# Kernel optimization log

Measured on AMD Instinct MI355X. Metric: run time of the kernel, lower is better.

## Reference

```python
import jax, jax.numpy as jnp
import numpy as np

N = 50000          # nodes
E = 1_600_000      # directed edges (before self loops)
G = 128            # graphs in batch
IN_F = 64
C1, H = 32, 4      # gat1: out_channels=32, heads=4 -> hidden 128
C2 = 64            # gat2: out_channels=64, heads=1, concat=False
OUT_F = 2
EPS = 1e-5
NEG_SLOPE = 0.2    # PyG GATv2Conv default


def setup_inputs() -> dict:
    key = jax.random.key(0)
    ks = jax.random.split(key, 24)
    s = 0.05
    inp = {
        'x': jax.random.normal(ks[0], (N, IN_F), jnp.float32),
        'edge_index': jax.random.randint(ks[1], (2, E), 0, N, dtype=jnp.int64),
        'batch': jnp.sort(jax.random.randint(ks[2], (N,), 0, G, dtype=jnp.int64)),
        # GATv2 layer 1 (in=64 -> 4 heads x 32)
        'W1l': jax.random.normal(ks[3], (IN_F, H * C1), jnp.float32) * s,
        'b1l': jnp.zeros((H * C1,), jnp.float32),
        'W1r': jax.random.normal(ks[4], (IN_F, H * C1), jnp.float32) * s,
        'b1r': jnp.zeros((H * C1,), jnp.float32),
        'att1': jax.random.normal(ks[5], (H, C1), jnp.float32) * s,
        'bias1': jnp.zeros((H * C1,), jnp.float32),
        # GATv2 layer 2 (in=128 -> 1 head x 64, no concat)
        'W2l': jax.random.normal(ks[6], (H * C1, C2), jnp.float32) * s,
        'b2l': jnp.zeros((C2,), jnp.float32),
        'W2r': jax.random.normal(ks[7], (H * C1, C2), jnp.float32) * s,
        'b2r': jnp.zeros((C2,), jnp.float32),
        'att2': jax.random.normal(ks[8], (1, C2), jnp.float32) * s,
        'bias2': jnp.zeros((C2,), jnp.float32),
        # batchnorms (batch-statistics normalization)
        'bn1_g': jnp.ones((H * C1,), jnp.float32),
        'bn1_b': jnp.zeros((H * C1,), jnp.float32),
        'bn2_g': jnp.ones((C2,), jnp.float32),
        'bn2_b': jnp.zeros((C2,), jnp.float32),
        # final linear: CL2_F*3 -> out_f
        'lin_w': jax.random.normal(ks[9], (3 * C2, OUT_F), jnp.float32) * s,
        'lin_b': jnp.zeros((OUT_F,), jnp.float32),
    }
    return inp


def _gatv2(x, Wl, bl, Wr, br, att, bias, src, dst, heads, ch, concat, n_nodes):
    # x: [N, F_in]; src/dst: [E'] (self loops already appended)
    xl = (x @ Wl + bl).reshape(n_nodes, heads, ch)  # source transform
    xr = (x @ Wr + br).reshape(n_nodes, heads, ch)  # target transform
    m = jax.nn.leaky_relu(xl[src] + xr[dst], NEG_SLOPE)      # [E', H, C]
    logits = jnp.einsum('ehc,hc->eh', m, att)                # [E', H]
    # segment softmax over destination nodes (every node has a self loop)
    mx = jax.ops.segment_max(logits, dst, num_segments=n_nodes)
    a = jnp.exp(logits - mx[dst])
    denom = jax.ops.segment_sum(a, dst, num_segments=n_nodes)
    alpha = a / denom[dst]                                   # [E', H]
    out = jax.ops.segment_sum(xl[src] * alpha[..., None], dst,
                              num_segments=n_nodes)          # [N, H, C]
    if concat:
        out = out.reshape(n_nodes, heads * ch)
    else:
        out = out.mean(axis=1)
    return out + bias


def _bn(h, gamma, beta):
    mu = h.mean(axis=0)
    var = h.var(axis=0)
    return (h - mu) * jax.lax.rsqrt(var + EPS) * gamma + beta


def reference(x, edge_index, batch, W1l, b1l, W1r, b1r, att1, bias1,
              W2l, b2l, W2r, b2r, att2, bias2,
              bn1_g, bn1_b, bn2_g, bn2_b, lin_w, lin_b):
    n = x.shape[0]
    loops = jnp.arange(n, dtype=edge_index.dtype)
    src = jnp.concatenate([edge_index[0], loops])  # PyG add_self_loops=True
    dst = jnp.concatenate([edge_index[1], loops])

    h = jax.nn.relu(_gatv2(x, W1l, b1l, W1r, b1r, att1, bias1,
                           src, dst, H, C1, True, n))
    h = _bn(h, bn1_g, bn1_b)      # dropout is identity (eval)
    h = jax.nn.relu(_gatv2(h, W2l, b2l, W2r, b2r, att2, bias2,
                           src, dst, 1, C2, False, n))
    h = _bn(h, bn2_g, bn2_b)

    x0 = jax.ops.segment_sum(h, batch, num_segments=G)                  # add pool
    cnt = jax.ops.segment_sum(jnp.ones((n, 1), h.dtype), batch, num_segments=G)
    x1 = x0 / jnp.maximum(cnt, 1.0)                                     # mean pool
    x2 = jax.ops.segment_max(h, batch, num_segments=G)                  # max pool
    feat = jnp.concatenate([x0, x1, x2], axis=-1)                       # [G, 3*C2]
    return feat @ lin_w + lin_b
```

## Files before the change

kernel.cpp:

```cpp
#include <hip/hip_runtime.h>
#include <hip/hip_fp16.h>
#include <math.h>

#define BSHIFT 7
#define CHUNK  8192
#define CAP    6144

__device__ inline __half2 habs2_(__half2 x){
  union { __half2 h; unsigned u; } c; c.h = x; c.u &= 0x7FFF7FFFu; return c.h;
}
__device__ inline __half2 lrelu2_(__half2 x, __half2 c06, __half2 c04){
  return __hfma2(c04, habs2_(x), __hmul2(c06, x));
}

__global__ __launch_bounds__(256) void k_pre(const int* __restrict__ ei, int E, int N, int NB,
    int* __restrict__ bfill, unsigned* __restrict__ ebuf,
    const float* __restrict__ X,
    const float* __restrict__ Wl, const float* __restrict__ bl,
    const float* __restrict__ Wr, const float* __restrict__ br,
    __half* __restrict__ outl, __half* __restrict__ outr, int bb){
  __shared__ float xs[32][64];
  if ((int)blockIdx.x < bb){
    int* hist = (int*)&xs[0][0];
    int base = blockIdx.x*CHUNK;
    int EL = E + N;
    int end = min(base + CHUNK, EL);
    for (int i = threadIdx.x; i < NB; i += 256) hist[i] = 0;
    __syncthreads();
    for (int e = base + threadIdx.x; e < end; e += 256){
      int d = (e < E) ? ei[E + e] : (e - E);
      atomicAdd(&hist[d >> BSHIFT], 1);
    }
    __syncthreads();
    for (int b = threadIdx.x; b < NB; b += 256){
      int c = hist[b];
      hist[b] = (c > 0) ? (b*CAP + atomicAdd(&bfill[b], c)) : 0;
    }
    __syncthreads();
    for (int e = base + threadIdx.x; e < end; e += 256){
      int s, d;
      if (e < E){ s = ei[e]; d = ei[E + e]; } else { s = d = e - E; }
      int pos = atomicAdd(&hist[d >> BSHIFT], 1);
      ebuf[pos] = (unsigned)s | ((unsigned)d << 16);
    }
  } else {
    const int tid = threadIdx.x;
    const int n0 = ((int)blockIdx.x - bb)*32;
    for (int t = tid; t < 32*64; t += 256){
      int r = t >> 6, c = t & 63;
      int node = n0 + r;
      xs[r][c] = (node < N) ? X[(size_t)node*64 + c] : 0.f;
    }
    __syncthreads();
    const int jg = tid & 63;
    const int ng = tid >> 6;
    const int q  = jg*4;
    const bool isL = (q < 128);
    const float* W = isL ? Wl : Wr;
    const int jj   = isL ? q : q - 128;
    const float* bbp = isL ? bl : br;
    __half* OUT    = isL ? outl : outr;
    const float4 bias4 = *(const float4*)(bbp + jj);
    float acc[8][4];
    #pragma unroll
    for (int n = 0; n < 8; ++n){ acc[n][0]=acc[n][1]=acc[n][2]=acc[n][3]=0.f; }
    for (int k = 0; k < 64; k += 4){
      const float4 w0 = *(const float4*)(W + (size_t)(k+0)*128 + jj);
      const float4 w1 = *(const float4*)(W + (size_t)(k+1)*128 + jj);
      const float4 w2 = *(const float4*)(W + (size_t)(k+2)*128 + jj);
      const float4 w3 = *(const float4*)(W + (size_t)(k+3)*128 + jj);
      #pragma unroll
      for (int n = 0; n < 8; ++n){
        const float4 xv = *(const float4*)(&xs[ng*8 + n][k]);
        acc[n][0] = fmaf(xv.w,w3.x, fmaf(xv.z,w2.x, fmaf(xv.y,w1.x, fmaf(xv.x,w0.x, acc[n][0]))));
        acc[n][1] = fmaf(xv.w,w3.y, fmaf(xv.z,w2.y, fmaf(xv.y,w1.y, fmaf(xv.x,w0.y, acc[n][1]))));
        acc[n][2] = fmaf(xv.w,w3.z, fmaf(xv.z,w2.z, fmaf(xv.y,w1.z, fmaf(xv.x,w0.z, acc[n][2]))));
        acc[n][3] = fmaf(xv.w,w3.w, fmaf(xv.z,w2.w, fmaf(xv.y,w1.w, fmaf(xv.x,w0.w, acc[n][3]))));
      }
    }
    #pragma unroll
    for (int n = 0; n < 8; ++n){
      int node = n0 + ng*8 + n;
      if (node < N){
        union { __half2 h[2]; uint2 u; } cv;
        cv.h[0] = __floats2half2_rn(acc[n][0]+bias4.x, acc[n][1]+bias4.y);
        cv.h[1] = __floats2half2_rn(acc[n][2]+bias4.z, acc[n][3]+bias4.w);
        *(uint2*)(OUT + (size_t)node*128 + jj) = cv.u;
      }
    }
  }
}

__global__ __launch_bounds__(1024) void k_fine(const unsigned* __restrict__ ebuf,
    const int* __restrict__ bfill, int N, int NB,
    int* __restrict__ rstart, int* __restrict__ rend, int* __restrict__ esrc){
  __shared__ int cnt[128];
  __shared__ int sc[128];
  __shared__ int base[128];
  int b = blockIdx.x;
  int n0 = b << BSHIFT;
  int nn = min(128, N - n0);
  int e0 = b*CAP;
  int e1 = e0 + bfill[b];
  if (threadIdx.x < 128) cnt[threadIdx.x] = 0;
  __syncthreads();
  for (int e = e0 + threadIdx.x; e < e1; e += 1024)
    atomicAdd(&cnt[(ebuf[e] >> 16) & 127], 1);
  __syncthreads();
  if (threadIdx.x < 128) sc[threadIdx.x] = cnt[threadIdx.x];
  __syncthreads();
  for (int off = 1; off < 128; off <<= 1){
    int v = 0;
    if (threadIdx.x < 128 && (int)threadIdx.x >= off) v = sc[threadIdx.x - off];
    __syncthreads();
    if (threadIdx.x < 128) sc[threadIdx.x] += v;
    __syncthreads();
  }
  if (threadIdx.x < 128){
    int bs = e0 + sc[threadIdx.x] - cnt[threadIdx.x];
    base[threadIdx.x] = bs;
    if ((int)threadIdx.x < nn){
      rstart[n0 + threadIdx.x] = bs;
      rend[n0 + threadIdx.x]   = bs + cnt[threadIdx.x];
    }
    cnt[threadIdx.x] = 0;
  }
  __syncthreads();
  for (int e = e0 + threadIdx.x; e < e1; e += 1024){
    unsigned pk = ebuf[e];
    int local = (int)(pk >> 16) & 127;
    int pos = base[local] + atomicAdd(&cnt[local], 1);
    esrc[pos] = (int)(pk & 0xffffu);
  }
}

__global__ __launch_bounds__(256) void k_gemm2(const __half2* __restrict__ X2,
    const float* __restrict__ Wl, const float* __restrict__ bl,
    const float* __restrict__ Wr, const float* __restrict__ br,
    __half* __restrict__ outl, __half* __restrict__ outr, int N,
    const float* __restrict__ bsum, const float* __restrict__ bsq,
    const float* __restrict__ gam, const float* __restrict__ bet){
  __shared__ float xs[32][128];
  const int tid = threadIdx.x;
  const int n0 = blockIdx.x*32;
  const float invN = 1.f/(float)N;
  for (int t = tid; t < 32*64; t += 256){
    int r = t >> 6, c2 = t & 63, c = c2*2;
    int node = n0 + r;
    float2 v = (node < N) ? __half22float2(X2[(size_t)node*64 + c2]) : make_float2(0.f,0.f);
    float m0 = bsum[c]*invN,   m1 = bsum[c+1]*invN;
    float r0 = rsqrtf(bsq[c]*invN   - m0*m0 + 1e-5f);
    float r1 = rsqrtf(bsq[c+1]*invN - m1*m1 + 1e-5f);
    v.x = (v.x - m0) * r0 * gam[c  ] + bet[c  ];
    v.y = (v.y - m1) * r1 * gam[c+1] + bet[c+1];
    xs[r][c] = v.x; xs[r][c+1] = v.y;
  }
  __syncthreads();
  const int jg = tid & 31;
  const int ng = tid >> 5;
  const int q  = jg*4;
  const bool isL = (q < 64);
  const float* W = isL ? Wl : Wr;
  const int jj   = isL ? q : q - 64;
  const float* bbp = isL ? bl : br;
  __half* OUT    = isL ? outl : outr;
  const float4 bias4 = *(const float4*)(bbp + jj);
  float acc[4][4];
  #pragma unroll
  for (int n = 0; n < 4; ++n){ acc[n][0]=acc[n][1]=acc[n][2]=acc[n][3]=0.f; }
  for (int k = 0; k < 128; k += 4){
    const float4 w0 = *(const float4*)(W + (size_t)(k+0)*64 + jj);
    const float4 w1 = *(const float4*)(W + (size_t)(k+1)*64 + jj);
    const float4 w2 = *(const float4*)(W + (size_t)(k+2)*64 + jj);
    const float4 w3 = *(const float4*)(W + (size_t)(k+3)*64 + jj);
    #pragma unroll
    for (int n = 0; n < 4; ++n){
      const float4 xv = *(const float4*)(&xs[ng*4 + n][k]);
      acc[n][0] = fmaf(xv.w,w3.x, fmaf(xv.z,w2.x, fmaf(xv.y,w1.x, fmaf(xv.x,w0.x, acc[n][0]))));
      acc[n][1] = fmaf(xv.w,w3.y, fmaf(xv.z,w2.y, fmaf(xv.y,w1.y, fmaf(xv.x,w0.y, acc[n][1]))));
      acc[n][2] = fmaf(xv.w,w3.z, fmaf(xv.z,w2.z, fmaf(xv.y,w1.z, fmaf(xv.x,w0.z, acc[n][2]))));
      acc[n][3] = fmaf(xv.w,w3.w, fmaf(xv.z,w2.w, fmaf(xv.y,w1.w, fmaf(xv.x,w0.w, acc[n][3]))));
    }
  }
  #pragma unroll
  for (int n = 0; n < 4; ++n){
    int node = n0 + ng*4 + n;
    if (node < N){
      union { __half2 h[2]; uint2 u; } cv;
      cv.h[0] = __floats2half2_rn(acc[n][0]+bias4.x, acc[n][1]+bias4.y);
      cv.h[1] = __floats2half2_rn(acc[n][2]+bias4.z, acc[n][3]+bias4.w);
      *(uint2*)(OUT + (size_t)node*64 + jj) = cv.u;
    }
  }
}

__global__ __launch_bounds__(256, 6) void k_gat1(const __half* __restrict__ xl, const __half* __restrict__ xr,
    const int* __restrict__ rstart, const int* __restrict__ rend,
    const int* __restrict__ esrc,
    const float* __restrict__ att, const float* __restrict__ bias,
    __half* __restrict__ h1, int N){
  int wv = (blockIdx.x*256 + threadIdx.x) >> 6;
  int lane = threadIdx.x & 63;
  int g = lane >> 4;
  int t = lane & 15;
  int node = wv*4 + g;
  bool live = node < N;
  int nd = live ? node : 0;
  int c0 = t*8;
  const __half2 c06 = __float2half2_rn(0.6f);
  const __half2 c04 = __float2half2_rn(0.4f);
  union { uint4 u; __half2 h[4]; } xru;
  xru.u = *(const uint4*)(xr + (size_t)nd*128 + c0);
  float4 a0 = *(const float4*)(att + c0);
  float4 a1 = *(const float4*)(att + c0 + 4);
  __half2 av2[4] = { __floats2half2_rn(a0.x,a0.y), __floats2half2_rn(a0.z,a0.w),
                     __floats2half2_rn(a1.x,a1.y), __floats2half2_rn(a1.z,a1.w) };
  int r0 = live ? rstart[nd] : 0;
  int r1 = live ? rend[nd]   : 0;
  int d  = r1 - r0;
  d = max(d, __shfl_xor(d, 16));
  d = max(d, __shfl_xor(d, 32));
  const char* xb = (const char*)xl;
  const unsigned cb = (unsigned)(c0*2);
  float s = 0.f;
  __half2 acc2[4];
  #pragma unroll
  for (int k = 0; k < 4; ++k) acc2[k] = __float2half2_rn(0.f);
  union V { uint4 u; __half2 h[4]; } cur[4], nxt[4];
  #pragma unroll
  for (int q = 0; q < 4; ++q){
    int e = r0 + q;
    unsigned j = (unsigned)esrc[e < r1 ? e : r0];
    cur[q].u = *(const uint4*)(xb + ((j << 8) + cb));
  }
  for (int i = 0; i < d; i += 4){
    #pragma unroll
    for (int q = 0; q < 4; ++q){
      int e = r0 + i + 4 + q;
      unsigned j = (unsigned)esrc[e < r1 ? e : r0];
      nxt[q].u = *(const uint4*)(xb + ((j << 8) + cb));
    }
    #pragma unroll
    for (int q = 0; q < 4; ++q){
      bool valid = (r0 + i + q) < r1;
      __half2 p2 = __float2half2_rn(0.f);
      #pragma unroll
      for (int k = 0; k < 4; ++k){
        __half2 m2 = __hadd2(cur[q].h[k], xru.h[k]);
        p2 = __hfma2(lrelu2_(m2, c06, c04), av2[k], p2);
      }
      float p = __low2float(p2) + __high2float(p2);
      p += __shfl_xor(p, 1);
      p += __shfl_xor(p, 2);
      float w = valid ? __expf(p) : 0.f;
      s += w;
      __half2 w2 = __float2half2_rn(w);
      #pragma unroll
      for (int k = 0; k < 4; ++k) acc2[k] = __hfma2(w2, cur[q].h[k], acc2[k]);
    }
    #pragma unroll
    for (int q = 0; q < 4; ++q) cur[q] = nxt[q];
  }
  if (live){
    float inv = 1.f/s;
    float4 b0 = *(const float4*)(bias + c0);
    float4 b1 = *(const float4*)(bias + c0 + 4);
    float bv[8] = {b0.x,b0.y,b0.z,b0.w,b1.x,b1.y,b1.z,b1.w};
    union { __half2 h[4]; uint4 u; } o;
    #pragma unroll
    for (int k = 0; k < 4; ++k){
      float2 af = __half22float2(acc2[k]);
      float f0 = fmaxf(af.x*inv + bv[2*k],   0.f);
      float f1 = fmaxf(af.y*inv + bv[2*k+1], 0.f);
      o.h[k] = __floats2half2_rn(f0, f1);
    }
    *(uint4*)(h1 + (size_t)nd*128 + c0) = o.u;
  }
}

__global__ __launch_bounds__(256, 6) void k_gat2(const __half* __restrict__ xl, const __half* __restrict__ xr,
    const int* __restrict__ rstart, const int* __restrict__ rend,
    const int* __restrict__ esrc,
    const float* __restrict__ att, const float* __restrict__ bias,
    __half* __restrict__ h2, int N){
  int wv = (blockIdx.x*256 + threadIdx.x) >> 6;
  int lane = threadIdx.x & 63;
  int g = lane >> 3;
  int t = lane & 7;
  int node = wv*8 + g;
  bool live = node < N;
  int nd = live ? node : 0;
  int c0 = t*8;
  const __half2 c06 = __float2half2_rn(0.6f);
  const __half2 c04 = __float2half2_rn(0.4f);
  union { uint4 u; __half2 h[4]; } xru;
  xru.u = *(const uint4*)(xr + (size_t)nd*64 + c0);
  float4 a0 = *(const float4*)(att + c0);
  float4 a1 = *(const float4*)(att + c0 + 4);
  __half2 av2[4] = { __floats2half2_rn(a0.x,a0.y), __floats2half2_rn(a0.z,a0.w),
                     __floats2half2_rn(a1.x,a1.y), __floats2half2_rn(a1.z,a1.w) };
  int r0 = live ? rstart[nd] : 0;
  int r1 = live ? rend[nd]   : 0;
  int d  = r1 - r0;
  d = max(d, __shfl_xor(d, 8));
  d = max(d, __shfl_xor(d, 16));
  d = max(d, __shfl_xor(d, 32));
  const char* xb = (const char*)xl;
  const unsigned cb = (unsigned)(c0*2);
  float s = 0.f;
  __half2 acc2[4];
  #pragma unroll
  for (int k = 0; k < 4; ++k) acc2[k] = __float2half2_rn(0.f);
  union V { uint4 u; __half2 h[4]; } cur[4], nxt[4];
  #pragma unroll
  for (int q = 0; q < 4; ++q){
    int e = r0 + q;
    unsigned j = (unsigned)esrc[e < r1 ? e : r0];
    cur[q].u = *(const uint4*)(xb + ((j << 7) + cb));
  }
  for (int i = 0; i < d; i += 4){
    #pragma unroll
    for (int q = 0; q < 4; ++q){
      int e = r0 + i + 4 + q;
      unsigned j = (unsigned)esrc[e < r1 ? e : r0];
      nxt[q].u = *(const uint4*)(xb + ((j << 7) + cb));
    }
    #pragma unroll
    for (int q = 0; q < 4; ++q){
      bool valid = (r0 + i + q) < r1;
      __half2 p2 = __float2half2_rn(0.f);
      #pragma unroll
      for (int k = 0; k < 4; ++k){
        __half2 m2 = __hadd2(cur[q].h[k], xru.h[k]);
        p2 = __hfma2(lrelu2_(m2, c06, c04), av2[k], p2);
      }
      float p = __low2float(p2) + __high2float(p2);
      p += __shfl_xor(p, 1);
      p += __shfl_xor(p, 2);
      p += __shfl_xor(p, 4);
      float w = valid ? __expf(p) : 0.f;
      s += w;
      __half2 w2 = __float2half2_rn(w);
      #pragma unroll
      for (int k = 0; k < 4; ++k) acc2[k] = __hfma2(w2, cur[q].h[k], acc2[k]);
    }
    #pragma unroll
    for (int q = 0; q < 4; ++q) cur[q] = nxt[q];
  }
  if (live){
    float inv = 1.f/s;
    float4 b0 = *(const float4*)(bias + c0);
    float4 b1 = *(const float4*)(bias + c0 + 4);
    float bv[8] = {b0.x,b0.y,b0.z,b0.w,b1.x,b1.y,b1.z,b1.w};
    union { __half2 h[4]; uint4 u; } o;
    #pragma unroll
    for (int k = 0; k < 4; ++k){
      float2 af = __half22float2(acc2[k]);
      float f0 = fmaxf(af.x*inv + bv[2*k],   0.f);
      float f1 = fmaxf(af.y*inv + bv[2*k+1], 0.f);
      o.h[k] = __floats2half2_rn(f0, f1);
    }
    *(uint4*)(h2 + (size_t)nd*64 + c0) = o.u;
  }
}

template<int C>
__global__ __launch_bounds__(256) void k_bnstats(const __half* __restrict__ h, int N,
    float* __restrict__ sum, float* __restrict__ sq){
  constexpr int RPB = 256/C;
  int c = threadIdx.x % C;
  int sub = threadIdx.x / C;
  float s = 0.f, q = 0.f;
  for (int r = blockIdx.x*RPB + sub; r < N; r += gridDim.x*RPB){
    float v = __half2float(h[(size_t)r*C + c]);
    s += v; q += v*v;
  }
  __shared__ float ls[256], lq[256];
  ls[threadIdx.x] = s; lq[threadIdx.x] = q;
  __syncthreads();
  if (threadIdx.x < C){
    float S = ls[c], Q = lq[c];
    #pragma unroll
    for (int u = 1; u < RPB; ++u){ S += ls[u*C + c]; Q += lq[u*C + c]; }
    atomicAdd(&sum[c], S);
    atomicAdd(&sq[c], Q);
  }
}

__global__ __launch_bounds__(256) void k_pool(const __half* __restrict__ h2, const int* __restrict__ batch, int N,
    const float* __restrict__ bsum, const float* __restrict__ bsq,
    const float* __restrict__ g, const float* __restrict__ b,
    const float* __restrict__ lw, const float* __restrict__ lb,
    float* __restrict__ out){
  int gr = blockIdx.x;
  int lo = 0, hi = N;
  while (lo < hi){ int mid = (lo+hi)>>1; if (batch[mid] < gr) lo = mid+1; else hi = mid; }
  int r0 = lo;
  lo = r0; hi = N;
  while (lo < hi){ int mid = (lo+hi)>>1; if (batch[mid] < gr+1) lo = mid+1; else hi = mid; }
  int r1 = lo;
  int c = threadIdx.x & 63;
  int sub = threadIdx.x >> 6;
  const float invN = 1.f/(float)N;
  float m = bsum[c]*invN;
  float rs = rsqrtf(bsq[c]*invN - m*m + 1e-5f);
  float aff_s = rs*g[c];
  float aff_b = b[c] - m*aff_s;
  float s = 0.f, mx = -INFINITY;
  for (int r = r0 + sub; r < r1; r += 4){
    float v = __half2float(h2[(size_t)r*64 + c])*aff_s + aff_b;
    s += v; mx = fmaxf(mx, v);
  }
  __shared__ float ls[256], lm[256], ft[192];
  ls[threadIdx.x] = s; lm[threadIdx.x] = mx;
  __syncthreads();
  if (threadIdx.x < 64){
    float S = ls[c] + ls[64+c] + ls[128+c] + ls[192+c];
    float M = fmaxf(fmaxf(lm[c], lm[64+c]), fmaxf(lm[128+c], lm[192+c]));
    float cnt = (float)max(r1 - r0, 1);
    ft[c]       = S;
    ft[64 + c]  = S/cnt;
    ft[128 + c] = M;
  }
  __syncthreads();
  if (threadIdx.x < 2){
    float acc = lb[threadIdx.x];
    #pragma unroll 4
    for (int k = 0; k < 192; ++k) acc += ft[k] * lw[k*2 + threadIdx.x];
    out[gr*2 + threadIdx.x] = acc;
  }
}

extern "C" void kernel_launch(void* const* d_in, const int* in_sizes, int n_in,
                              void* d_out, int out_size, void* d_ws, size_t ws_size,
                              hipStream_t stream) {
  const float* x    = (const float*)d_in[0];
  const int*   ei   = (const int*)d_in[1];
  const int*   batch= (const int*)d_in[2];
  const float* W1l  = (const float*)d_in[3];
  const float* b1l  = (const float*)d_in[4];
  const float* W1r  = (const float*)d_in[5];
  const float* b1r  = (const float*)d_in[6];
  const float* att1 = (const float*)d_in[7];
  const float* bias1= (const float*)d_in[8];
  const float* W2l  = (const float*)d_in[9];
  const float* b2l  = (const float*)d_in[10];
  const float* W2r  = (const float*)d_in[11];
  const float* b2r  = (const float*)d_in[12];
  const float* att2 = (const float*)d_in[13];
  const float* bias2= (const float*)d_in[14];
  const float* g1   = (const float*)d_in[15];
  const float* be1  = (const float*)d_in[16];
  const float* g2   = (const float*)d_in[17];
  const float* be2  = (const float*)d_in[18];
  const float* lw   = (const float*)d_in[19];
  const float* lb   = (const float*)d_in[20];

  const int N  = in_sizes[0] / 64;
  const int E  = in_sizes[1] / 2;
  const int EL = E + N;
  const int G  = 128;
  const int NB = (N + 127) >> BSHIFT;

  char* p = (char*)d_ws;
  auto carve = [&](size_t bytes)->char*{ char* r = p; p += (bytes + 255) & ~(size_t)255; return r; };
  int* zero   = (int*)carve((size_t)(NB + 384)*4);
  int* bfill  = zero;
  float* stats = (float*)(zero + NB);
  float* bn1_sum = stats;
  float* bn1_sq  = stats + 128;
  float* bn2_sum = stats + 256;
  float* bn2_sq  = stats + 320;
  int* rstart = (int*)carve((size_t)N*4);
  int* rend   = (int*)carve((size_t)N*4);
  unsigned* ebuf = (unsigned*)carve((size_t)NB*CAP*4);
  int* esrc   = (int*)carve((size_t)NB*CAP*4);
  __half* xl1 = (__half*)carve((size_t)N*128*2);
  __half* xr1 = (__half*)carve((size_t)N*128*2);
  __half* h1  = (__half*)carve((size_t)N*128*2);
  __half* xl2 = xl1;
  __half* xr2 = xl1 + (size_t)N*64;
  __half* h2  = xr1;

  hipMemsetAsync(zero, 0, (size_t)(NB + 384)*4, stream);

  const int bb = (EL + CHUNK - 1)/CHUNK;
  const int gb = (N + 31)/32;
  k_pre<<<bb + gb, 256, 0, stream>>>(ei, E, N, NB, bfill, ebuf,
                                     x, W1l, b1l, W1r, b1r, xl1, xr1, bb);
  k_fine<<<NB, 1024, 0, stream>>>(ebuf, bfill, N, NB, rstart, rend, esrc);

  const int nb1 = ((N + 3)/4*64 + 255)/256;
  const int nb2 = ((N + 7)/8*64 + 255)/256;
  k_gat1<<<nb1, 256, 0, stream>>>(xl1, xr1, rstart, rend, esrc, att1, bias1, h1, N);
  k_bnstats<128><<<256, 256, 0, stream>>>(h1, N, bn1_sum, bn1_sq);
  k_gemm2<<<gb, 256, 0, stream>>>((const __half2*)h1, W2l, b2l, W2r, b2r, xl2, xr2, N,
                                  bn1_sum, bn1_sq, g1, be1);
  k_gat2<<<nb2, 256, 0, stream>>>(xl2, xr2, rstart, rend, esrc, att2, bias2, h2, N);
  k_bnstats<64><<<256, 256, 0, stream>>>(h2, N, bn2_sum, bn2_sq);
  k_pool<<<G, 256, 0, stream>>>(h2, batch, N, bn2_sum, bn2_sq, g2, be2, lw, lb, (float*)d_out);
}
```

Before: 367.5 us.

## Sort destination nodes by degree to balance GAT wave work

Adds a degree histogram, scan and permutation pass that orders nodes by descending in-degree, and makes both GAT aggregation kernels process nodes through this permutation. Nodes sharing a wavefront then have similar degrees, so less time is spent on lanes idling while the wave loops to the group's maximum degree. Edge-index loads drop their bounds clamp and read past the row end into padded esrc, masking the index to 16 bits. The cost is three extra small launches, an indirection load per node, and scattered output writes and xr reads.

```diff
diff --git a/kernel.cpp b/kernel.cpp
--- a/kernel.cpp
+++ b/kernel.cpp
@@ -131,6 +131,73 @@
     int local = (int)(pk >> 16) & 127;
     int pos = base[local] + atomicAdd(&cnt[local], 1);
     esrc[pos] = (int)(pk & 0xffffu);
+  }
+}
+
+__global__ __launch_bounds__(256) void k_dhist(const int* __restrict__ rstart, const int* __restrict__ rend,
+                                               int N, int* __restrict__ dh){
+  __shared__ int h[512];
+  for (int i = threadIdx.x; i < 512; i += 256) h[i] = 0;
+  __syncthreads();
+  #pragma unroll
+  for (int k = 0; k < 4; ++k){
+    int n = blockIdx.x*1024 + k*256 + threadIdx.x;
+    if (n < N){
+      int deg = rend[n] - rstart[n];
+      atomicAdd(&h[511 - min(deg, 511)], 1);
+    }
+  }
+  __syncthreads();
+  for (int i = threadIdx.x; i < 512; i += 256){
+    int c = h[i];
+    if (c) atomicAdd(&dh[i], c);
+  }
+}
+
+__global__ __launch_bounds__(512) void k_dscan(const int* __restrict__ dh, int* __restrict__ dfill){
+  __shared__ int s[512];
+  int tid = threadIdx.x;
+  int v = dh[tid];
+  s[tid] = v; __syncthreads();
+  for (int off = 1; off < 512; off <<= 1){
+    int t = (tid >= off) ? s[tid - off] : 0;
+    __syncthreads();
+    s[tid] += t;
+    __syncthreads();
+  }
+  dfill[tid] = s[tid] - v;
+}
+
+__global__ __launch_bounds__(256) void k_dperm(const int* __restrict__ rstart, const int* __restrict__ rend,
+                                               int N, int* __restrict__ dfill, int* __restrict__ perm){
+  __shared__ int h[512];
+  __shared__ int mybin[1024];
+  int base_n = blockIdx.x*1024;
+  for (int i = threadIdx.x; i < 512; i += 256) h[i] = 0;
+  __syncthreads();
+  #pragma unroll
+  for (int k = 0; k < 4; ++k){
+    int n = base_n + k*256 + threadIdx.x;
+    if (n < N){
+      int deg = rend[n] - rstart[n];
+      int b = 511 - min(deg, 511);
+      mybin[k*256 + threadIdx.x] = b;
+      atomicAdd(&h[b], 1);
+    }
+  }
+  __syncthreads();
+  for (int i = threadIdx.x; i < 512; i += 256){
+    int c = h[i];
+    h[i] = c ? atomicAdd(&dfill[i], c) : 0;
+  }
+  __syncthreads();
+  #pragma unroll
+  for (int k = 0; k < 4; ++k){
+    int n = base_n + k*256 + threadIdx.x;
+    if (n < N){
+      int pos = atomicAdd(&h[mybin[k*256 + threadIdx.x]], 1);
+      perm[pos] = n;
+    }
   }
 }
 
@@ -196,16 +263,16 @@
 
 __global__ __launch_bounds__(256, 6) void k_gat1(const __half* __restrict__ xl, const __half* __restrict__ xr,
     const int* __restrict__ rstart, const int* __restrict__ rend,
-    const int* __restrict__ esrc,
+    const int* __restrict__ esrc, const int* __restrict__ perm,
     const float* __restrict__ att, const float* __restrict__ bias,
     __half* __restrict__ h1, int N){
   int wv = (blockIdx.x*256 + threadIdx.x) >> 6;
   int lane = threadIdx.x & 63;
   int g = lane >> 4;
   int t = lane & 15;
-  int node = wv*4 + g;
-  bool live = node < N;
-  int nd = live ? node : 0;
+  int idx = wv*4 + g;
+  bool live = idx < N;
+  int nd = perm[min(idx, N-1)];
   int c0 = t*8;
   const __half2 c06 = __float2half2_rn(0.6f);
   const __half2 c04 = __float2half2_rn(0.4f);
@@ -215,8 +282,8 @@
   float4 a1 = *(const float4*)(att + c0 + 4);
   __half2 av2[4] = { __floats2half2_rn(a0.x,a0.y), __floats2half2_rn(a0.z,a0.w),
                      __floats2half2_rn(a1.x,a1.y), __floats2half2_rn(a1.z,a1.w) };
-  int r0 = live ? rstart[nd] : 0;
-  int r1 = live ? rend[nd]   : 0;
+  int r0 = rstart[nd];
+  int r1 = rend[nd];
   int d  = r1 - r0;
   d = max(d, __shfl_xor(d, 16));
   d = max(d, __shfl_xor(d, 32));
@@ -229,15 +296,13 @@
   union V { uint4 u; __half2 h[4]; } cur[4], nxt[4];
   #pragma unroll
   for (int q = 0; q < 4; ++q){
-    int e = r0 + q;
-    unsigned j = (unsigned)esrc[e < r1 ? e : r0];
+    unsigned j = (unsigned)esrc[r0 + q] & 0xFFFFu;
     cur[q].u = *(const uint4*)(xb + ((j << 8) + cb));
   }
   for (int i = 0; i < d; i += 4){
     #pragma unroll
     for (int q = 0; q < 4; ++q){
-      int e = r0 + i + 4 + q;
-      unsigned j = (unsigned)esrc[e < r1 ? e : r0];
+      unsigned j = (unsigned)esrc[r0 + i + 4 + q] & 0xFFFFu;
       nxt[q].u = *(const uint4*)(xb + ((j << 8) + cb));
     }
     #pragma unroll
@@ -280,16 +345,16 @@
 
 __global__ __launch_bounds__(256, 6) void k_gat2(const __half* __restrict__ xl, const __half* __restrict__ xr,
     const int* __restrict__ rstart, const int* __restrict__ rend,
-    const int* __restrict__ esrc,
+    const int* __restrict__ esrc, const int* __restrict__ perm,
     const float* __restrict__ att, const float* __restrict__ bias,
     __half* __restrict__ h2, int N){
   int wv = (blockIdx.x*256 + threadIdx.x) >> 6;
   int lane = threadIdx.x & 63;
   int g = lane >> 3;
   int t = lane & 7;
-  int node = wv*8 + g;
-  bool live = node < N;
-  int nd = live ? node : 0;
+  int idx = wv*8 + g;
+  bool live = idx < N;
+  int nd = perm[min(idx, N-1)];
   int c0 = t*8;
   const __half2 c06 = __float2half2_rn(0.6f);
   const __half2 c04 = __float2half2_rn(0.4f);
@@ -299,8 +364,8 @@
   float4 a1 = *(const float4*)(att + c0 + 4);
   __half2 av2[4] = { __floats2half2_rn(a0.x,a0.y), __floats2half2_rn(a0.z,a0.w),
                      __floats2half2_rn(a1.x,a1.y), __floats2half2_rn(a1.z,a1.w) };
-  int r0 = live ? rstart[nd] : 0;
-  int r1 = live ? rend[nd]   : 0;
+  int r0 = rstart[nd];
+  int r1 = rend[nd];
   int d  = r1 - r0;
   d = max(d, __shfl_xor(d, 8));
   d = max(d, __shfl_xor(d, 16));
@@ -314,15 +379,13 @@
   union V { uint4 u; __half2 h[4]; } cur[4], nxt[4];
   #pragma unroll
   for (int q = 0; q < 4; ++q){
-    int e = r0 + q;
-    unsigned j = (unsigned)esrc[e < r1 ? e : r0];
+    unsigned j = (unsigned)esrc[r0 + q] & 0xFFFFu;
     cur[q].u = *(const uint4*)(xb + ((j << 7) + cb));
   }
   for (int i = 0; i < d; i += 4){
     #pragma unroll
     for (int q = 0; q < 4; ++q){
-      int e = r0 + i + 4 + q;
-      unsigned j = (unsigned)esrc[e < r1 ? e : r0];
+      unsigned j = (unsigned)esrc[r0 + i + 4 + q] & 0xFFFFu;
       nxt[q].u = *(const uint4*)(xb + ((j << 7) + cb));
     }
     #pragma unroll
@@ -464,17 +527,20 @@
 
   char* p = (char*)d_ws;
   auto carve = [&](size_t bytes)->char*{ char* r = p; p += (bytes + 255) & ~(size_t)255; return r; };
-  int* zero   = (int*)carve((size_t)(NB + 384)*4);
+  int* zero   = (int*)carve((size_t)(NB + 512 + 384)*4);
   int* bfill  = zero;
-  float* stats = (float*)(zero + NB);
+  int* dh     = zero + NB;
+  float* stats = (float*)(zero + NB + 512);
   float* bn1_sum = stats;
   float* bn1_sq  = stats + 128;
   float* bn2_sum = stats + 256;
   float* bn2_sq  = stats + 320;
+  int* dfill  = (int*)carve((size_t)512*4);
   int* rstart = (int*)carve((size_t)N*4);
   int* rend   = (int*)carve((size_t)N*4);
+  int* perm   = (int*)carve((size_t)N*4);
   unsigned* ebuf = (unsigned*)carve((size_t)NB*CAP*4);
-  int* esrc   = (int*)carve((size_t)NB*CAP*4);
+  int* esrc   = (int*)carve((size_t)(NB*CAP + 1024)*4);
   __half* xl1 = (__half*)carve((size_t)N*128*2);
   __half* xr1 = (__half*)carve((size_t)N*128*2);
   __half* h1  = (__half*)carve((size_t)N*128*2);
@@ -482,21 +548,25 @@
   __half* xr2 = xl1 + (size_t)N*64;
   __half* h2  = xr1;
 
-  hipMemsetAsync(zero, 0, (size_t)(NB + 384)*4, stream);
+  hipMemsetAsync(zero, 0, (size_t)(NB + 512 + 384)*4, stream);
 
   const int bb = (EL + CHUNK - 1)/CHUNK;
   const int gb = (N + 31)/32;
+  const int db = (N + 1023)/1024;
   k_pre<<<bb + gb, 256, 0, stream>>>(ei, E, N, NB, bfill, ebuf,
                                      x, W1l, b1l, W1r, b1r, xl1, xr1, bb);
   k_fine<<<NB, 1024, 0, stream>>>(ebuf, bfill, N, NB, rstart, rend, esrc);
+  k_dhist<<<db, 256, 0, stream>>>(rstart, rend, N, dh);
+  k_dscan<<<1, 512, 0, stream>>>(dh, dfill);
+  k_dperm<<<db, 256, 0, stream>>>(rstart, rend, N, dfill, perm);
 
   const int nb1 = ((N + 3)/4*64 + 255)/256;
   const int nb2 = ((N + 7)/8*64 + 255)/256;
-  k_gat1<<<nb1, 256, 0, stream>>>(xl1, xr1, rstart, rend, esrc, att1, bias1, h1, N);
+  k_gat1<<<nb1, 256, 0, stream>>>(xl1, xr1, rstart, rend, esrc, perm, att1, bias1, h1, N);
   k_bnstats<128><<<256, 256, 0, stream>>>(h1, N, bn1_sum, bn1_sq);
   k_gemm2<<<gb, 256, 0, stream>>>((const __half2*)h1, W2l, b2l, W2r, b2r, xl2, xr2, N,
                                   bn1_sum, bn1_sq, g1, be1);
-  k_gat2<<<nb2, 256, 0, stream>>>(xl2, xr2, rstart, rend, esrc, att2, bias2, h2, N);
+  k_gat2<<<nb2, 256, 0, stream>>>(xl2, xr2, rstart, rend, esrc, perm, att2, bias2, h2, N);
   k_bnstats<64><<<256, 256, 0, stream>>>(h2, N, bn2_sum, bn2_sq);
   k_pool<<<G, 256, 0, stream>>>(h2, batch, N, bn2_sum, bn2_sq, g2, be2, lw, lb, (float*)d_out);
 }
```

Result: no change. 369.4 us (+0.5%).
